# Performance work log

Hardware: AMD Instinct MI355X
Metric: run time of the kernel (lower is better)

## Reference

```python
import jax, jax.numpy as jnp
import numpy as np

SOFTMAX_SCALE = 10.0  # self.softmax_scale
EPS = 1e-4


def _patches(img, k=3):
    # img: [H, W, C] -> patches laid out as conv filters [k, k, C, L], L = H*W
    # (matches tf.image.extract_patches SAME/stride1 + reshape + transpose([0,2,3,4,1]))
    H, W, C = img.shape
    pad = (k - 1) // 2
    xp = jnp.pad(img, ((pad, pad), (pad, pad), (0, 0)))
    pat = jnp.stack([jnp.stack([xp[p:p + H, q:q + W] for q in range(k)]) for p in range(k)])
    # pat: [k, k, H, W, C] -> [k, k, C, H*W]; L index is row-major (h*W + w) like TF reshape
    return pat.transpose(0, 1, 4, 2, 3).reshape(k, k, C, H * W)


def _normed(p):
    # per-patch L2 normalization over the k*k*C axes (axes 0,1,2)
    return p / jnp.maximum(jnp.sqrt(jnp.sum(p * p, axis=(0, 1, 2))), EPS)


def _corr_recon(a, b, k=3):
    # a, b: [H', W', C] shifted feature maps
    Hp, Wp, C = a.shape
    L = Hp * Wp
    pa = _patches(a, k)  # [k,k,C,L]
    pb = _patches(b, k)
    y = (_normed(pa) * _normed(pb)).reshape(k * k * C, L)
    att = y.T @ y                                   # [L, L] patch-correlation scores
    att = jax.nn.softmax(att.reshape(1, Hp, Wp, L) * SOFTMAX_SCALE, axis=3)
    dn = ('NHWC', 'HWIO', 'NHWC')
    # tf.nn.conv2d_transpose(att, filters=[k,k,C,L], stride=1, SAME); rate=1 so /rate**2 is a no-op
    ya = jax.lax.conv_transpose(att, pa, (1, 1), 'SAME', dimension_numbers=dn, transpose_kernel=True)[0]
    yb = jax.lax.conv_transpose(att, pb, (1, 1), 'SAME', dimension_numbers=dn, transpose_kernel=True)[0]
    return ya, yb  # each [H', W', C]


def _ecattn_single(xi):
    # xi: [H, W, C]
    left, right = xi[:-1], xi[1:]          # vertical neighbor pair, [H-1, W, C]
    top, bottom = xi[:, 1:], xi[:, :-1]    # horizontal neighbor pair, [H, W-1, C]
    yl, yr = _corr_recon(left, right)
    ylr = jnp.concatenate([yr[:1], (yr[1:] + yl[:-1]) * 0.5, yl[-1:]], axis=0)   # [H, W, C]
    yt, yb = _corr_recon(top, bottom)
    ytb = jnp.concatenate([yt[:, :1], (yt[:, 1:] + yb[:, :-1]) * 0.5, yb[:, -1:]], axis=1)  # [H, W, C]
    return (ylr + ytb) * 0.5


def setup_inputs() -> dict:
    key = jax.random.key(0)
    k1, k2 = jax.random.split(key)
    B, H, W, C = 4, 32, 32, 256
    x = jax.random.normal(k1, (B, H, W, C), dtype=jnp.float32)
    mask = jax.random.uniform(k2, (B, H, W, 1), dtype=jnp.float32)
    return {'x': x, 'mask': mask}


def reference(x, mask):
    # mask is accepted by the layer's call() but unused inside contextualAttention
    return jax.vmap(_ecattn_single)(x)
```

## Files before the change

### kernel.cpp

```cpp
#include <hip/hip_runtime.h>


typedef _Float16 half8 __attribute__((ext_vector_type(8)));
typedef _Float16 half8u __attribute__((ext_vector_type(8), aligned(4)));
typedef _Float16 half4h __attribute__((ext_vector_type(4)));
typedef _Float16 half4u __attribute__((ext_vector_type(4), aligned(8)));
typedef float floatx4 __attribute__((ext_vector_type(4)));

constexpr int NL = 992, NC = 256, NC2 = 512;
constexpr int NLL = NL * NL;
constexpr int OFF_ABT = 0;
constexpr int OFF_MH  = OFF_ABT + NL * NC2 / 2;
constexpr int OFF_SA  = OFF_MH + NL * NC / 2;
constexpr int OFF_SB  = OFF_SA + 1024;
constexpr int OFF_INV = OFF_SA + 2048;
constexpr int OFF_Y   = OFF_SA + 3072;
constexpr int OFF_B0  = OFF_Y + NL * NC2 / 2;
constexpr int OFF_B1  = OFF_B0 + NLL / 2;
constexpr int TSTRIDE = OFF_B1 + NLL / 2;

__device__ __forceinline__ void gload16(const void* g, void* l) {
    __builtin_amdgcn_global_load_lds(
        (const __attribute__((address_space(1))) unsigned int*)g,
        (__attribute__((address_space(3))) unsigned int*)(unsigned long)(uintptr_t)l,
        16, 0, 0);
}

__global__ __launch_bounds__(256) void k_stage(const float* __restrict__ x,
                                               float* __restrict__ ws) {
    const int t = blockIdx.x & 7;
    const int l0 = (blockIdx.x >> 3) * 32;
    const int s = t >> 1, o = t & 1;
    float* wst = ws + (size_t)t * TSTRIDE;
    _Float16* __restrict__ ABt = (_Float16*)(wst + OFF_ABT);
    _Float16* __restrict__ Mh = (_Float16*)(wst + OFF_MH);
    __shared__ float Ta[32 * 33], Tb[32 * 33];
    const int tid = threadIdx.x;
    const int li = tid >> 3, cq = tid & 7;
    const int l = l0 + li;
    int aoff, boff;
    if (o == 0) {
        const int lh = l >> 5, lw = l & 31;
        aoff = ((s * 32 + lh) * 32 + lw) * NC;
        boff = aoff + 32 * NC;
    } else {
        const int lh = l / 31, lw = l - lh * 31;
        boff = ((s * 32 + lh) * 32 + lw) * NC;
        aoff = boff + NC;
    }
    float sa = 0.0f, sb = 0.0f;
    for (int cc = 0; cc < 8; ++cc) {
        const int c0 = cc * 32;
        const float4 a4 = *(const float4*)&x[aoff + c0 + cq * 4];
        const float4 b4 = *(const float4*)&x[boff + c0 + cq * 4];
        half4h m;
        m[0] = (_Float16)(a4.x * b4.x); m[1] = (_Float16)(a4.y * b4.y);
        m[2] = (_Float16)(a4.z * b4.z); m[3] = (_Float16)(a4.w * b4.w);
        *(half4u*)&Mh[l * NC + c0 + cq * 4] = m;
        sa += a4.x * a4.x + a4.y * a4.y + a4.z * a4.z + a4.w * a4.w;
        sb += b4.x * b4.x + b4.y * b4.y + b4.z * b4.z + b4.w * b4.w;
        __syncthreads();
        Ta[(cq * 4 + 0) * 33 + li] = a4.x; Tb[(cq * 4 + 0) * 33 + li] = b4.x;
        Ta[(cq * 4 + 1) * 33 + li] = a4.y; Tb[(cq * 4 + 1) * 33 + li] = b4.y;
        Ta[(cq * 4 + 2) * 33 + li] = a4.z; Tb[(cq * 4 + 2) * 33 + li] = b4.z;
        Ta[(cq * 4 + 3) * 33 + li] = a4.w; Tb[(cq * 4 + 3) * 33 + li] = b4.w;
        __syncthreads();
        const int ci = li, lq = cq;
        half4h ha, hb;
#pragma unroll
        for (int j = 0; j < 4; ++j) {
            ha[j] = (_Float16)Ta[ci * 33 + lq * 4 + j];
            hb[j] = (_Float16)Tb[ci * 33 + lq * 4 + j];
        }
        *(half4u*)&ABt[(c0 + ci) * NL + l0 + lq * 4] = ha;
        *(half4u*)&ABt[(NC + c0 + ci) * NL + l0 + lq * 4] = hb;
    }
#pragma unroll
    for (int off = 4; off > 0; off >>= 1) {
        sa += __shfl_down(sa, off, 8);
        sb += __shfl_down(sb, off, 8);
    }
    if (cq == 0) {
        wst[OFF_SA + l] = sa;
        wst[OFF_SB + l] = sb;
    }
}

__global__ __launch_bounds__(256) void k_gram(float* __restrict__ ws) {
    const int t = blockIdx.x & 7;
    const int u = blockIdx.x >> 3;
    const int i0 = (u >> 4) * 64, j0 = (u & 15) * 64;
    float* wst = ws + (size_t)t * TSTRIDE;
    const _Float16* __restrict__ M = (const _Float16*)(wst + OFF_MH);
    _Float16* __restrict__ S = (_Float16*)(wst + OFF_B0);
    const int tid = threadIdx.x;

    if (u == 0) {
        const int o = t & 1;
        const int Hp = o ? 32 : 31, Wp = o ? 31 : 32;
#pragma unroll
        for (int q = 0; q < 4; ++q) {
            const int l = tid + q * 256;
            if (l < NL) {
                const int h = l / Wp, w = l - h * Wp;
                float na2 = 0.0f, nb2 = 0.0f;
#pragma unroll
                for (int dh = -1; dh <= 1; ++dh)
#pragma unroll
                    for (int dw = -1; dw <= 1; ++dw) {
                        const int hh = h + dh, ww = w + dw;
                        if ((unsigned)hh < (unsigned)Hp && (unsigned)ww < (unsigned)Wp) {
                            const int ll = hh * Wp + ww;
                            na2 += wst[OFF_SA + ll];
                            nb2 += wst[OFF_SB + ll];
                        }
                    }
                const float na = fmaxf(sqrtf(na2), 1e-4f);
                const float nb = fmaxf(sqrtf(nb2), 1e-4f);
                wst[OFF_INV + l] = 1.0f / (na * nb);
            }
        }
    }

    __shared__ __align__(16) _Float16 As[64 * 64];
    __shared__ __align__(16) _Float16 Bs[64 * 64];
    const int wave = tid >> 6, lane = tid & 63;
    const int wm = wave & 1, wn = wave >> 1;
    const int l15 = lane & 15, quad = lane >> 4;
    floatx4 acc[2][2] = {};
    for (int k0 = 0; k0 < NC; k0 += 64) {
        __syncthreads();
#pragma unroll
        for (int rr = 0; rr < 2; ++rr) {
            const int slot = tid + rr * 256;
            const int row = slot >> 3, cg = (slot & 7) * 8;
            if (i0 + row < NL) gload16(&M[(i0 + row) * NC + k0 + cg], &As[row * 64 + cg]);
            if (j0 + row < NL) gload16(&M[(j0 + row) * NC + k0 + cg], &Bs[row * 64 + cg]);
        }
        __syncthreads();
#pragma unroll
        for (int kk = 0; kk < 2; ++kk) {
            half8 a[2], b[2];
#pragma unroll
            for (int mt = 0; mt < 2; ++mt) a[mt] = *(const half8*)&As[(wm * 32 + mt * 16 + l15) * 64 + kk * 32 + quad * 8];
#pragma unroll
            for (int nt = 0; nt < 2; ++nt) b[nt] = *(const half8*)&Bs[(wn * 32 + nt * 16 + l15) * 64 + kk * 32 + quad * 8];
#pragma unroll
            for (int mt = 0; mt < 2; ++mt)
#pragma unroll
                for (int nt = 0; nt < 2; ++nt)
                    acc[mt][nt] = __builtin_amdgcn_mfma_f32_16x16x32_f16(a[mt], b[nt], acc[mt][nt], 0, 0, 0);
        }
    }
#pragma unroll
    for (int mt = 0; mt < 2; ++mt)
#pragma unroll
        for (int nt = 0; nt < 2; ++nt)
#pragma unroll
            for (int r = 0; r < 4; ++r) {
                const int row = i0 + wm * 32 + mt * 16 + quad * 4 + r;
                const int col = j0 + wn * 32 + nt * 16 + l15;
                if (row < NL && col < NL) S[row * NL + col] = (_Float16)acc[mt][nt][r];
            }
}

template<int WP, int HP>
__device__ __forceinline__ void softmax9_body(float* __restrict__ wst,
                                              const int l1, const int tid) {
    const _Float16* __restrict__ S = (const _Float16*)(wst + OFF_B0);
    const float* __restrict__ inv = wst + OFF_INV;
    _Float16* __restrict__ Ph = (_Float16*)(wst + OFF_B1);
    const int c0 = tid * 4;
    const int h1 = l1 / WP, w1 = l1 % WP;
    float e[4] = {0.f, 0.f, 0.f, 0.f};
    float sum = 0.0f;
    if (tid < 248) {
        int hc[4], wc[4];
#pragma unroll
        for (int j = 0; j < 4; ++j) { hc[j] = (c0 + j) / WP; wc[j] = (c0 + j) % WP; }
        float g[4] = {0.f, 0.f, 0.f, 0.f};
        const _Float16* base = S + l1 * NL + c0;
#pragma unroll
        for (int dh = -1; dh <= 1; ++dh) {
            const bool oh1 = (unsigned)(h1 + dh) < (unsigned)HP;
#pragma unroll
            for (int dw = -1; dw <= 1; ++dw) {
                const int sh = dh * WP + dw;
                const int par = sh & 1;
                const bool ok1 = oh1 && (unsigned)(w1 + dw) < (unsigned)WP;
                const half8u v = *(const half8u*)(base + sh * (NL + 1) - par);
#pragma unroll
                for (int j = 0; j < 4; ++j) {
                    const bool ok = ok1 && (unsigned)(hc[j] + dh) < (unsigned)HP &&
                                           (unsigned)(wc[j] + dw) < (unsigned)WP;
                    if (ok) g[j] += (float)v[j + par];
                }
            }
        }
        const float inv1 = inv[l1] * 10.0f;
#pragma unroll
        for (int j = 0; j < 4; ++j) {
            e[j] = __expf(g[j] * inv1 * inv[c0 + j]);
            sum += e[j];
        }
    }
    __shared__ float red[4];
    const int wave = tid >> 6, lane = tid & 63;
#pragma unroll
    for (int off = 32; off > 0; off >>= 1) sum += __shfl_down(sum, off);
    if (lane == 0) red[wave] = sum;
    __syncthreads();
    sum = red[0] + red[1] + red[2] + red[3];
    const float rs = 1.0f / sum;
    if (tid < 248) {
        half4h o;
#pragma unroll
        for (int j = 0; j < 4; ++j) o[j] = (_Float16)(e[j] * rs);
        *(half4u*)(Ph + l1 * NL + c0) = o;
    }
}

__global__ __launch_bounds__(256) void k_softmax9(float* __restrict__ ws) {
    const int t = blockIdx.x & 7;
    const int l1 = blockIdx.x >> 3;
    float* wst = ws + (size_t)t * TSTRIDE;
    if (t & 1) softmax9_body<31, 32>(wst, l1, threadIdx.x);
    else       softmax9_body<32, 31>(wst, l1, threadIdx.x);
}

template<int WP, int HP>
__device__ __forceinline__ void band9p_body(float* __restrict__ wst,
                                            const int m, const int tid) {
    if (tid >= 248) return;
    const _Float16* __restrict__ P = (const _Float16*)(wst + OFF_B1);
    _Float16* __restrict__ W = (_Float16*)(wst + OFF_B0);
    const int c0 = tid * 4;
    const int hm = m / WP, wm = m % WP;
    int hc[4], wc[4];
#pragma unroll
    for (int j = 0; j < 4; ++j) { hc[j] = (c0 + j) / WP; wc[j] = (c0 + j) % WP; }
    float acc[4] = {0.f, 0.f, 0.f, 0.f};
    const _Float16* base = P + m * NL + c0;
#pragma unroll
    for (int dh = -1; dh <= 1; ++dh) {
        const bool oh1 = (unsigned)(hm + dh) < (unsigned)HP;
#pragma unroll
        for (int dw = -1; dw <= 1; ++dw) {
            const int sh = dh * WP + dw;
            const int par = sh & 1;
            const bool ok1 = oh1 && (unsigned)(wm + dw) < (unsigned)WP;
            const half8u v = *(const half8u*)(base + sh * (NL + 1) - par);
#pragma unroll
            for (int j = 0; j < 4; ++j) {
                const bool ok = ok1 && (unsigned)(hc[j] + dh) < (unsigned)HP &&
                                       (unsigned)(wc[j] + dw) < (unsigned)WP;
                if (ok) acc[j] += (float)v[j + par];
            }
        }
    }
    half4h o;
#pragma unroll
    for (int j = 0; j < 4; ++j) o[j] = (_Float16)acc[j];
    *(half4u*)(W + m * NL + c0) = o;
}

__global__ __launch_bounds__(256) void k_band9p(float* __restrict__ ws) {
    const int t = blockIdx.x & 7;
    const int m = blockIdx.x >> 3;
    float* wst = ws + (size_t)t * TSTRIDE;
    if (t & 1) band9p_body<31, 32>(wst, m, threadIdx.x);
    else       band9p_body<32, 31>(wst, m, threadIdx.x);
}

__global__ __launch_bounds__(256) void k_recon(float* __restrict__ ws) {
    const int t = blockIdx.x & 7;
    const int u = blockIdx.x >> 3;
    const int i0 = (u >> 3) * 64, j0 = (u & 7) * 64;
    float* wst = ws + (size_t)t * TSTRIDE;
    const _Float16* __restrict__ Wm = (const _Float16*)(wst + OFF_B0);
    const _Float16* __restrict__ ABt = (const _Float16*)(wst + OFF_ABT);
    _Float16* __restrict__ Y = (_Float16*)(wst + OFF_Y);
    __shared__ __align__(16) _Float16 As[64 * 32];
    __shared__ __align__(16) _Float16 Bs[64 * 32];
    const int tid = threadIdx.x;
    const int wave = tid >> 6, lane = tid & 63;
    const int wm = wave & 1, wn = wave >> 1;
    const int l15 = lane & 15, quad = lane >> 4;
    floatx4 acc[2][2] = {};
    const int row = tid >> 2, cg = (tid & 3) * 8;
    for (int k0 = 0; k0 < NL; k0 += 32) {
        __syncthreads();
        if (i0 + row < NL) gload16(&Wm[(i0 + row) * NL + k0 + cg], &As[row * 32 + cg]);
        gload16(&ABt[(j0 + row) * NL + k0 + cg], &Bs[row * 32 + cg]);
        __syncthreads();
        half8 a[2], b[2];
#pragma unroll
        for (int mt = 0; mt < 2; ++mt) a[mt] = *(const half8*)&As[(wm * 32 + mt * 16 + l15) * 32 + quad * 8];
#pragma unroll
        for (int nt = 0; nt < 2; ++nt) b[nt] = *(const half8*)&Bs[(wn * 32 + nt * 16 + l15) * 32 + quad * 8];
#pragma unroll
        for (int mt = 0; mt < 2; ++mt)
#pragma unroll
            for (int nt = 0; nt < 2; ++nt)
                acc[mt][nt] = __builtin_amdgcn_mfma_f32_16x16x32_f16(a[mt], b[nt], acc[mt][nt], 0, 0, 0);
    }
#pragma unroll
    for (int mt = 0; mt < 2; ++mt)
#pragma unroll
        for (int nt = 0; nt < 2; ++nt)
#pragma unroll
            for (int r = 0; r < 4; ++r) {
                const int rw = i0 + wm * 32 + mt * 16 + quad * 4 + r;
                const int col = j0 + wn * 32 + nt * 16 + l15;
                if (rw < NL) Y[rw * NC2 + col] = (_Float16)acc[mt][nt][r];
            }
}

__global__ __launch_bounds__(256) void k_combine(float* __restrict__ out,
                                                 const float* __restrict__ ws) {
    const int idx = blockIdx.x;
    const int s = idx >> 10;
    const int hw = idx & 1023;
    const int h = hw >> 5, w = hw & 31;
    const int c = threadIdx.x;
    const _Float16* Ylr = (const _Float16*)(ws + (size_t)(2 * s) * TSTRIDE + OFF_Y);
    const _Float16* Ytb = (const _Float16*)(ws + (size_t)(2 * s + 1) * TSTRIDE + OFF_Y);
    float v = 0.0f;
    if (h < 31) v += (float)Ylr[(h * 32 + w) * NC2 + NC + c] * (h == 0 ? 1.0f : 0.5f);
    if (h >= 1) v += (float)Ylr[((h - 1) * 32 + w) * NC2 + c] * (h == 31 ? 1.0f : 0.5f);
    if (w < 31) v += (float)Ytb[(h * 31 + w) * NC2 + c] * (w == 0 ? 1.0f : 0.5f);
    if (w >= 1) v += (float)Ytb[(h * 31 + (w - 1)) * NC2 + NC + c] * (w == 31 ? 1.0f : 0.5f);
    out[(size_t)idx * NC + c] = v * 0.5f;
}

extern "C" void kernel_launch(void* const* d_in, const int* in_sizes, int n_in,
                              void* d_out, int out_size, void* d_ws, size_t ws_size,
                              hipStream_t stream) {
    const float* x = (const float*)d_in[0];
    float* out = (float*)d_out;
    float* ws = (float*)d_ws;

    hipLaunchKernelGGL(k_stage,    dim3(8 * 31),  dim3(256), 0, stream, x, ws);
    hipLaunchKernelGGL(k_gram,     dim3(8 * 256), dim3(256), 0, stream, ws);
    hipLaunchKernelGGL(k_softmax9, dim3(8 * NL),  dim3(256), 0, stream, ws);
    hipLaunchKernelGGL(k_band9p,   dim3(8 * NL),  dim3(256), 0, stream, ws);
    hipLaunchKernelGGL(k_recon,    dim3(8 * 128), dim3(256), 0, stream, ws);
    hipLaunchKernelGGL(k_combine,  dim3(4096),    dim3(256), 0, stream, out, ws);
}
```

Measured before the change: 144.4 us.

## Pad recon K dimension to 1024 and double the K tile per barrier

Pads the ABt and band-weight matrices to a 1024-element row stride and zero-fills the tail, so the recon GEMM can step through K in 64-wide tiles. Each barrier pair then covers two MFMA sub-steps, halving the synchronizations in the inner loop. The staging kernel also double-buffers its transpose scratch, which removes one __syncthreads per channel chunk. The cost is extra zero writes, slightly more workspace, and twice the LDS per recon block, which may reduce occupancy.

Measured after the change: 146.3 us. About the same (+1.3%).

```diff
diff --git a/kernel.cpp b/kernel.cpp
--- a/kernel.cpp
+++ b/kernel.cpp
@@ -7,16 +7,16 @@
 typedef _Float16 half4u __attribute__((ext_vector_type(4), aligned(8)));
 typedef float floatx4 __attribute__((ext_vector_type(4)));
 
-constexpr int NL = 992, NC = 256, NC2 = 512;
+constexpr int NL = 992, NLP = 1024, NC = 256, NC2 = 512;
 constexpr int NLL = NL * NL;
 constexpr int OFF_ABT = 0;
-constexpr int OFF_MH  = OFF_ABT + NL * NC2 / 2;
+constexpr int OFF_MH  = OFF_ABT + NC2 * NLP / 2;
 constexpr int OFF_SA  = OFF_MH + NL * NC / 2;
 constexpr int OFF_SB  = OFF_SA + 1024;
 constexpr int OFF_INV = OFF_SA + 2048;
 constexpr int OFF_Y   = OFF_SA + 3072;
 constexpr int OFF_B0  = OFF_Y + NL * NC2 / 2;
-constexpr int OFF_B1  = OFF_B0 + NLL / 2;
+constexpr int OFF_B1  = OFF_B0 + NL * NLP / 2;
 constexpr int TSTRIDE = OFF_B1 + NLL / 2;
 
 __device__ __forceinline__ void gload16(const void* g, void* l) {
@@ -34,7 +34,7 @@
     float* wst = ws + (size_t)t * TSTRIDE;
     _Float16* __restrict__ ABt = (_Float16*)(wst + OFF_ABT);
     _Float16* __restrict__ Mh = (_Float16*)(wst + OFF_MH);
-    __shared__ float Ta[32 * 33], Tb[32 * 33];
+    __shared__ float Ta[2][32 * 33], Tb[2][32 * 33];
     const int tid = threadIdx.x;
     const int li = tid >> 3, cq = tid & 7;
     const int l = l0 + li;
@@ -48,9 +48,11 @@
         boff = ((s * 32 + lh) * 32 + lw) * NC;
         aoff = boff + NC;
     }
+    const half4h zero4 = {(_Float16)0.f, (_Float16)0.f, (_Float16)0.f, (_Float16)0.f};
     float sa = 0.0f, sb = 0.0f;
     for (int cc = 0; cc < 8; ++cc) {
         const int c0 = cc * 32;
+        const int pb = cc & 1;
         const float4 a4 = *(const float4*)&x[aoff + c0 + cq * 4];
         const float4 b4 = *(const float4*)&x[boff + c0 + cq * 4];
         half4h m;
@@ -59,21 +61,24 @@
         *(half4u*)&Mh[l * NC + c0 + cq * 4] = m;
         sa += a4.x * a4.x + a4.y * a4.y + a4.z * a4.z + a4.w * a4.w;
         sb += b4.x * b4.x + b4.y * b4.y + b4.z * b4.z + b4.w * b4.w;
-        __syncthreads();
-        Ta[(cq * 4 + 0) * 33 + li] = a4.x; Tb[(cq * 4 + 0) * 33 + li] = b4.x;
-        Ta[(cq * 4 + 1) * 33 + li] = a4.y; Tb[(cq * 4 + 1) * 33 + li] = b4.y;
-        Ta[(cq * 4 + 2) * 33 + li] = a4.z; Tb[(cq * 4 + 2) * 33 + li] = b4.z;
-        Ta[(cq * 4 + 3) * 33 + li] = a4.w; Tb[(cq * 4 + 3) * 33 + li] = b4.w;
+        Ta[pb][(cq * 4 + 0) * 33 + li] = a4.x; Tb[pb][(cq * 4 + 0) * 33 + li] = b4.x;
+        Ta[pb][(cq * 4 + 1) * 33 + li] = a4.y; Tb[pb][(cq * 4 + 1) * 33 + li] = b4.y;
+        Ta[pb][(cq * 4 + 2) * 33 + li] = a4.z; Tb[pb][(cq * 4 + 2) * 33 + li] = b4.z;
+        Ta[pb][(cq * 4 + 3) * 33 + li] = a4.w; Tb[pb][(cq * 4 + 3) * 33 + li] = b4.w;
         __syncthreads();
         const int ci = li, lq = cq;
         half4h ha, hb;
 #pragma unroll
         for (int j = 0; j < 4; ++j) {
-            ha[j] = (_Float16)Ta[ci * 33 + lq * 4 + j];
-            hb[j] = (_Float16)Tb[ci * 33 + lq * 4 + j];
-        }
-        *(half4u*)&ABt[(c0 + ci) * NL + l0 + lq * 4] = ha;
-        *(half4u*)&ABt[(NC + c0 + ci) * NL + l0 + lq * 4] = hb;
+            ha[j] = (_Float16)Ta[pb][ci * 33 + lq * 4 + j];
+            hb[j] = (_Float16)Tb[pb][ci * 33 + lq * 4 + j];
+        }
+        *(half4u*)&ABt[(c0 + ci) * NLP + l0 + lq * 4] = ha;
+        *(half4u*)&ABt[(NC + c0 + ci) * NLP + l0 + lq * 4] = hb;
+        if (l0 == 960) {
+            *(half4u*)&ABt[(c0 + ci) * NLP + 992 + lq * 4] = zero4;
+            *(half4u*)&ABt[(NC + c0 + ci) * NLP + 992 + lq * 4] = zero4;
+        }
     }
 #pragma unroll
     for (int off = 4; off > 0; off >>= 1) {
@@ -231,9 +236,13 @@
 template<int WP, int HP>
 __device__ __forceinline__ void band9p_body(float* __restrict__ wst,
                                             const int m, const int tid) {
-    if (tid >= 248) return;
+    _Float16* __restrict__ W = (_Float16*)(wst + OFF_B0);
+    if (tid >= 248) {
+        const half4h z = {(_Float16)0.f, (_Float16)0.f, (_Float16)0.f, (_Float16)0.f};
+        *(half4u*)(W + m * NLP + 992 + (tid - 248) * 4) = z;
+        return;
+    }
     const _Float16* __restrict__ P = (const _Float16*)(wst + OFF_B1);
-    _Float16* __restrict__ W = (_Float16*)(wst + OFF_B0);
     const int c0 = tid * 4;
     const int hm = m / WP, wm = m % WP;
     int hc[4], wc[4];
@@ -261,7 +270,7 @@
     half4h o;
 #pragma unroll
     for (int j = 0; j < 4; ++j) o[j] = (_Float16)acc[j];
-    *(half4u*)(W + m * NL + c0) = o;
+    *(half4u*)(W + m * NLP + c0) = o;
 }
 
 __global__ __launch_bounds__(256) void k_band9p(float* __restrict__ ws) {
@@ -280,29 +289,36 @@
     const _Float16* __restrict__ Wm = (const _Float16*)(wst + OFF_B0);
     const _Float16* __restrict__ ABt = (const _Float16*)(wst + OFF_ABT);
     _Float16* __restrict__ Y = (_Float16*)(wst + OFF_Y);
-    __shared__ __align__(16) _Float16 As[64 * 32];
-    __shared__ __align__(16) _Float16 Bs[64 * 32];
+    __shared__ __align__(16) _Float16 As[64 * 64];
+    __shared__ __align__(16) _Float16 Bs[64 * 64];
     const int tid = threadIdx.x;
     const int wave = tid >> 6, lane = tid & 63;
     const int wm = wave & 1, wn = wave >> 1;
     const int l15 = lane & 15, quad = lane >> 4;
     floatx4 acc[2][2] = {};
-    const int row = tid >> 2, cg = (tid & 3) * 8;
-    for (int k0 = 0; k0 < NL; k0 += 32) {
-        __syncthreads();
-        if (i0 + row < NL) gload16(&Wm[(i0 + row) * NL + k0 + cg], &As[row * 32 + cg]);
-        gload16(&ABt[(j0 + row) * NL + k0 + cg], &Bs[row * 32 + cg]);
-        __syncthreads();
-        half8 a[2], b[2];
-#pragma unroll
-        for (int mt = 0; mt < 2; ++mt) a[mt] = *(const half8*)&As[(wm * 32 + mt * 16 + l15) * 32 + quad * 8];
-#pragma unroll
-        for (int nt = 0; nt < 2; ++nt) b[nt] = *(const half8*)&Bs[(wn * 32 + nt * 16 + l15) * 32 + quad * 8];
-#pragma unroll
-        for (int mt = 0; mt < 2; ++mt)
-#pragma unroll
-            for (int nt = 0; nt < 2; ++nt)
-                acc[mt][nt] = __builtin_amdgcn_mfma_f32_16x16x32_f16(a[mt], b[nt], acc[mt][nt], 0, 0, 0);
+    for (int k0 = 0; k0 < NLP; k0 += 64) {
+        __syncthreads();
+#pragma unroll
+        for (int rr = 0; rr < 2; ++rr) {
+            const int slot = tid + rr * 256;
+            const int row = slot >> 3, cg = (slot & 7) * 8;
+            if (i0 + row < NL) gload16(&Wm[(i0 + row) * NLP + k0 + cg], &As[row * 64 + cg]);
+            gload16(&ABt[(j0 + row) * NLP + k0 + cg], &Bs[row * 64 + cg]);
+        }
+        __syncthreads();
+#pragma unroll
+        for (int kk = 0; kk < 2; ++kk) {
+            half8 a[2], b[2];
+#pragma unroll
+            for (int mt = 0; mt < 2; ++mt) a[mt] = *(const half8*)&As[(wm * 32 + mt * 16 + l15) * 64 + kk * 32 + quad * 8];
+#pragma unroll
+            for (int nt = 0; nt < 2; ++nt) b[nt] = *(const half8*)&Bs[(wn * 32 + nt * 16 + l15) * 64 + kk * 32 + quad * 8];
+#pragma unroll
+            for (int mt = 0; mt < 2; ++mt)
+#pragma unroll
+                for (int nt = 0; nt < 2; ++nt)
+                    acc[mt][nt] = __builtin_amdgcn_mfma_f32_16x16x32_f16(a[mt], b[nt], acc[mt][nt], 0, 0, 0);
+        }
     }
 #pragma unroll
     for (int mt = 0; mt < 2; ++mt)
```

## Store score and probability matrices in zero-padded 2D spatial layout

Applied to the files above, without the earlier changes.

Gram output and softmax probabilities are now written with columns in a zero-padded 34-wide spatial grid (row stride 1156) instead of a dense 992-wide layout. The 3x3 band-sum stencils in softmax and band kernels can then drop per-element boundary checks and only test the row-side offset, because out-of-range neighbours read padding zeros. The cost is extra zero-fill writes of padding cells, a slightly larger workspace, and scalar stores for the 31-wide case.

After: 156.6 us. +8.4%, slower.

```diff
diff --git a/kernel.cpp b/kernel.cpp
--- a/kernel.cpp
+++ b/kernel.cpp
@@ -4,11 +4,12 @@
 typedef _Float16 half8 __attribute__((ext_vector_type(8)));
 typedef _Float16 half8u __attribute__((ext_vector_type(8), aligned(4)));
 typedef _Float16 half4h __attribute__((ext_vector_type(4)));
+typedef _Float16 half4a __attribute__((ext_vector_type(4), aligned(4)));
 typedef _Float16 half4u __attribute__((ext_vector_type(4), aligned(8)));
 typedef float floatx4 __attribute__((ext_vector_type(4)));
 
 constexpr int NL = 992, NC = 256, NC2 = 512;
-constexpr int NLL = NL * NL;
+constexpr int ST = 34, PST = 1156;
 constexpr int OFF_ABT = 0;
 constexpr int OFF_MH  = OFF_ABT + NL * NC2 / 2;
 constexpr int OFF_SA  = OFF_MH + NL * NC / 2;
@@ -16,8 +17,8 @@
 constexpr int OFF_INV = OFF_SA + 2048;
 constexpr int OFF_Y   = OFF_SA + 3072;
 constexpr int OFF_B0  = OFF_Y + NL * NC2 / 2;
-constexpr int OFF_B1  = OFF_B0 + NLL / 2;
-constexpr int TSTRIDE = OFF_B1 + NLL / 2;
+constexpr int OFF_B1  = OFF_B0 + NL * PST / 2;
+constexpr int TSTRIDE = OFF_B1 + NL * PST / 2;
 
 __device__ __forceinline__ void gload16(const void* g, void* l) {
     __builtin_amdgcn_global_load_lds(
@@ -86,31 +87,27 @@
     }
 }
 
-__global__ __launch_bounds__(256) void k_gram(float* __restrict__ ws) {
-    const int t = blockIdx.x & 7;
-    const int u = blockIdx.x >> 3;
-    const int i0 = (u >> 4) * 64, j0 = (u & 15) * 64;
-    float* wst = ws + (size_t)t * TSTRIDE;
+template<int WP, int HP>
+__device__ __forceinline__ void gram_body(float* __restrict__ wst,
+                                          const int u, const int tid) {
     const _Float16* __restrict__ M = (const _Float16*)(wst + OFF_MH);
     _Float16* __restrict__ S = (_Float16*)(wst + OFF_B0);
-    const int tid = threadIdx.x;
+    const int i0 = (u >> 4) * 64, j0 = (u & 15) * 64;
 
     if (u == 0) {
-        const int o = t & 1;
-        const int Hp = o ? 32 : 31, Wp = o ? 31 : 32;
 #pragma unroll
         for (int q = 0; q < 4; ++q) {
             const int l = tid + q * 256;
             if (l < NL) {
-                const int h = l / Wp, w = l - h * Wp;
+                const int h = l / WP, w = l - h * WP;
                 float na2 = 0.0f, nb2 = 0.0f;
 #pragma unroll
                 for (int dh = -1; dh <= 1; ++dh)
 #pragma unroll
                     for (int dw = -1; dw <= 1; ++dw) {
                         const int hh = h + dh, ww = w + dw;
-                        if ((unsigned)hh < (unsigned)Hp && (unsigned)ww < (unsigned)Wp) {
-                            const int ll = hh * Wp + ww;
+                        if ((unsigned)hh < (unsigned)HP && (unsigned)ww < (unsigned)WP) {
+                            const int ll = hh * WP + ww;
                             na2 += wst[OFF_SA + ll];
                             nb2 += wst[OFF_SB + ll];
                         }
@@ -121,6 +118,19 @@
             }
         }
     }
+    {
+        const int rs = (u * 31) >> 3, re = ((u + 1) * 31) >> 3;
+        for (int r = rs; r < re; ++r)
+            for (int c = tid; c < PST; c += 256) {
+                bool real = false;
+                if (c >= ST + 2) {
+                    const int h = (c - 2) / ST - 1;
+                    const int w = (c - 2) % ST;
+                    real = (h < HP) && (w < WP);
+                }
+                if (!real) S[r * PST + c] = (_Float16)0.f;
+            }
+    }
 
     __shared__ __align__(16) _Float16 As[64 * 64];
     __shared__ __align__(16) _Float16 Bs[64 * 64];
@@ -155,13 +165,24 @@
 #pragma unroll
     for (int mt = 0; mt < 2; ++mt)
 #pragma unroll
-        for (int nt = 0; nt < 2; ++nt)
+        for (int nt = 0; nt < 2; ++nt) {
+            const int col = j0 + wn * 32 + nt * 16 + l15;
+            const int h2 = col / WP, w2 = col - h2 * WP;
+            const int pc = (h2 + 1) * ST + w2 + 2;
 #pragma unroll
             for (int r = 0; r < 4; ++r) {
                 const int row = i0 + wm * 32 + mt * 16 + quad * 4 + r;
-                const int col = j0 + wn * 32 + nt * 16 + l15;
-                if (row < NL && col < NL) S[row * NL + col] = (_Float16)acc[mt][nt][r];
-            }
+                if (row < NL && col < NL) S[row * PST + pc] = (_Float16)acc[mt][nt][r];
+            }
+        }
+}
+
+__global__ __launch_bounds__(256) void k_gram(float* __restrict__ ws) {
+    const int t = blockIdx.x & 7;
+    const int u = blockIdx.x >> 3;
+    float* wst = ws + (size_t)t * TSTRIDE;
+    if (t & 1) gram_body<31, 32>(wst, u, threadIdx.x);
+    else       gram_body<32, 31>(wst, u, threadIdx.x);
 }
 
 template<int WP, int HP>
@@ -170,38 +191,38 @@
     const _Float16* __restrict__ S = (const _Float16*)(wst + OFF_B0);
     const float* __restrict__ inv = wst + OFF_INV;
     _Float16* __restrict__ Ph = (_Float16*)(wst + OFF_B1);
-    const int c0 = tid * 4;
+    const int r2 = tid >> 3;
+    const int wq = (tid & 7) * 4;
     const int h1 = l1 / WP, w1 = l1 % WP;
+    const bool active = (r2 < HP);
+    const int p2 = (r2 + 1) * ST + wq + 2;
     float e[4] = {0.f, 0.f, 0.f, 0.f};
     float sum = 0.0f;
-    if (tid < 248) {
-        int hc[4], wc[4];
-#pragma unroll
-        for (int j = 0; j < 4; ++j) { hc[j] = (c0 + j) / WP; wc[j] = (c0 + j) % WP; }
+    if (active) {
+        const _Float16* base = S + l1 * PST + p2;
         float g[4] = {0.f, 0.f, 0.f, 0.f};
-        const _Float16* base = S + l1 * NL + c0;
 #pragma unroll
         for (int dh = -1; dh <= 1; ++dh) {
-            const bool oh1 = (unsigned)(h1 + dh) < (unsigned)HP;
+            const bool okh = (unsigned)(h1 + dh) < (unsigned)HP;
 #pragma unroll
             for (int dw = -1; dw <= 1; ++dw) {
-                const int sh = dh * WP + dw;
-                const int par = sh & 1;
-                const bool ok1 = oh1 && (unsigned)(w1 + dw) < (unsigned)WP;
-                const half8u v = *(const half8u*)(base + sh * (NL + 1) - par);
-#pragma unroll
-                for (int j = 0; j < 4; ++j) {
-                    const bool ok = ok1 && (unsigned)(hc[j] + dh) < (unsigned)HP &&
-                                           (unsigned)(wc[j] + dw) < (unsigned)WP;
-                    if (ok) g[j] += (float)v[j + par];
+                if (okh && (unsigned)(w1 + dw) < (unsigned)WP) {
+                    const int ro = (dh * WP + dw) * PST + dh * ST + dw;
+                    const int par = dw & 1;
+                    const half8u v = *(const half8u*)(base + ro - par);
+#pragma unroll
+                    for (int j = 0; j < 4; ++j) g[j] += (float)v[j + par];
                 }
             }
         }
         const float inv1 = inv[l1] * 10.0f;
 #pragma unroll
         for (int j = 0; j < 4; ++j) {
-            e[j] = __expf(g[j] * inv1 * inv[c0 + j]);
-            sum += e[j];
+            const int w = wq + j;
+            const int l2 = r2 * WP + w;
+            const float ee = (w < WP) ? __expf(g[j] * inv1 * inv[l2]) : 0.0f;
+            e[j] = ee;
+            sum += ee;
         }
     }
     __shared__ float red[4];
@@ -212,11 +233,20 @@
     __syncthreads();
     sum = red[0] + red[1] + red[2] + red[3];
     const float rs = 1.0f / sum;
-    if (tid < 248) {
+    if (active) {
         half4h o;
 #pragma unroll
         for (int j = 0; j < 4; ++j) o[j] = (_Float16)(e[j] * rs);
-        *(half4u*)(Ph + l1 * NL + c0) = o;
+        *(half4a*)(Ph + l1 * PST + p2) = o;
+    }
+    for (int c = tid; c < PST; c += 256) {
+        bool real = false;
+        if (c >= ST + 2) {
+            const int h = (c - 2) / ST - 1;
+            const int w = (c - 2) % ST;
+            real = (h < HP) && (w < WP);
+        }
+        if (!real) Ph[l1 * PST + c] = (_Float16)0.f;
     }
 }
 
@@ -231,37 +261,40 @@
 template<int WP, int HP>
 __device__ __forceinline__ void band9p_body(float* __restrict__ wst,
                                             const int m, const int tid) {
-    if (tid >= 248) return;
     const _Float16* __restrict__ P = (const _Float16*)(wst + OFF_B1);
     _Float16* __restrict__ W = (_Float16*)(wst + OFF_B0);
-    const int c0 = tid * 4;
+    const int r2 = tid >> 3;
+    const int wq = (tid & 7) * 4;
+    if (r2 >= HP) return;
     const int hm = m / WP, wm = m % WP;
-    int hc[4], wc[4];
-#pragma unroll
-    for (int j = 0; j < 4; ++j) { hc[j] = (c0 + j) / WP; wc[j] = (c0 + j) % WP; }
+    const int p2 = (r2 + 1) * ST + wq + 2;
+    const _Float16* base = P + m * PST + p2;
     float acc[4] = {0.f, 0.f, 0.f, 0.f};
-    const _Float16* base = P + m * NL + c0;
 #pragma unroll
     for (int dh = -1; dh <= 1; ++dh) {
-        const bool oh1 = (unsigned)(hm + dh) < (unsigned)HP;
+        const bool okh = (unsigned)(hm + dh) < (unsigned)HP;
 #pragma unroll
         for (int dw = -1; dw <= 1; ++dw) {
-            const int sh = dh * WP + dw;
-            const int par = sh & 1;
-            const bool ok1 = oh1 && (unsigned)(wm + dw) < (unsigned)WP;
-            const half8u v = *(const half8u*)(base + sh * (NL + 1) - par);
-#pragma unroll
-            for (int j = 0; j < 4; ++j) {
-                const bool ok = ok1 && (unsigned)(hc[j] + dh) < (unsigned)HP &&
-                                       (unsigned)(wc[j] + dw) < (unsigned)WP;
-                if (ok) acc[j] += (float)v[j + par];
-            }
-        }
-    }
-    half4h o;
-#pragma unroll
-    for (int j = 0; j < 4; ++j) o[j] = (_Float16)acc[j];
-    *(half4u*)(W + m * NL + c0) = o;
+            if (okh && (unsigned)(wm + dw) < (unsigned)WP) {
+                const int ro = (dh * WP + dw) * PST + dh * ST + dw;
+                const int par = dw & 1;
+                const half8u v = *(const half8u*)(base + ro - par);
+#pragma unroll
+                for (int j = 0; j < 4; ++j) acc[j] += (float)v[j + par];
+            }
+        }
+    }
+    const int c = r2 * WP + wq;
+    if (WP == 32) {
+        half4h o;
+#pragma unroll
+        for (int j = 0; j < 4; ++j) o[j] = (_Float16)acc[j];
+        *(half4a*)(W + m * NL + c) = o;
+    } else {
+#pragma unroll
+        for (int j = 0; j < 4; ++j)
+            if (wq + j < WP) W[m * NL + c + j] = (_Float16)acc[j];
+    }
 }
 
 __global__ __launch_bounds__(256) void k_band9p(float* __restrict__ ws) {
```
